# Kernel optimization log

Measured on AMD Instinct MI355X. Metric: run time of the kernel, lower is better.

Reference implementation:

```python
import jax, jax.numpy as jnp
import numpy as np

NUM_HEADS = 12


def _build_mask(N, unseen_size, dtype):
    # Columns for the last `unseen_size` tokens are masked (-inf) for every
    # query row EXCEPT the diagonal entries in that block (each unseen token
    # may attend to itself). Matches the original Python-loop construction.
    idx = jnp.arange(N)
    col_unseen = idx[None, :] >= (N - unseen_size)
    off_diag = idx[:, None] != idx[None, :]
    return jnp.where(col_unseen & off_diag, -jnp.inf, jnp.asarray(0.0, dtype))


def reference(x, w_qkv, w_proj, b_proj, unseen_size):
    B, N, C = x.shape
    H = NUM_HEADS
    d = C // H
    scale = d ** -0.5
    # qkv: (B,N,3C) -> (3,B,H,N,d)
    qkv = (x @ w_qkv.T).reshape(B, N, 3, H, d).transpose(2, 0, 3, 1, 4)
    q, k, v = qkv[0], qkv[1], qkv[2]
    attn = jnp.einsum('bhqd,bhkd->bhqk', q, k) * scale
    attn = attn + _build_mask(N, unseen_size, attn.dtype)  # broadcast (N,N)
    attn = jax.nn.softmax(attn, axis=-1)
    out = jnp.einsum('bhqk,bhkd->bhqd', attn, v)
    out = out.transpose(0, 2, 1, 3).reshape(B, N, C)
    return out @ w_proj.T + b_proj


def setup_inputs() -> dict:
    key = jax.random.key(0)
    k1, k2, k3 = jax.random.split(key, 3)
    B, N, C = 2, 2048, 768
    x = jax.random.normal(k1, (B, N, C), dtype=jnp.float32)
    w_qkv = jax.random.normal(k2, (3 * C, C), dtype=jnp.float32) * (C ** -0.5)
    w_proj = jax.random.normal(k3, (C, C), dtype=jnp.float32) * (C ** -0.5)
    b_proj = jnp.zeros((C,), dtype=jnp.float32)
    return {"x": x, "w_qkv": w_qkv, "w_proj": w_proj, "b_proj": b_proj,
            "unseen_size": 512}
```

## Files before the change

kernel.cpp:

```cpp
#include <hip/hip_runtime.h>
#include <math.h>

#define NH 12
#define DH 64
#define NSEQ 2048
#define NB 2
#define CDIM 768
#define NVIS 1536

typedef _Float16 half8 __attribute__((ext_vector_type(8)));
typedef _Float16 half4 __attribute__((ext_vector_type(4)));
typedef float floatx4 __attribute__((ext_vector_type(4)));

static constexpr size_t SZ_X    = (size_t)NB*NSEQ*CDIM;
static constexpr size_t SZ_WQKV = (size_t)3*CDIM*CDIM;
static constexpr size_t SZ_WP   = (size_t)CDIM*CDIM;
static constexpr size_t SZ_HEAD = (size_t)NB*NH*NSEQ*DH;

#define GLOAD_LDS16(gp, lp) \
  __builtin_amdgcn_global_load_lds((const __attribute__((address_space(1))) void*)(gp), \
                                   (__attribute__((address_space(3))) void*)(lp), 16, 0, 0)

__global__ __launch_bounds__(256) void convert_kernel(
    const float* __restrict__ x, const float* __restrict__ wqkv, const float* __restrict__ wp,
    _Float16* __restrict__ xb, _Float16* __restrict__ wqkvb, _Float16* __restrict__ wpb)
{
  size_t idx = ((size_t)blockIdx.x*256 + threadIdx.x)*4;
  const float* src; _Float16* dst; size_t off;
  if (idx < SZ_X)                        { src = x;    dst = xb;    off = idx; }
  else if (idx < SZ_X+SZ_WQKV)           { src = wqkv; dst = wqkvb; off = idx - SZ_X; }
  else if (idx < SZ_X+SZ_WQKV+SZ_WP)     { src = wp;   dst = wpb;   off = idx - SZ_X - SZ_WQKV; }
  else return;
  float4 v = *reinterpret_cast<const float4*>(src + off);
  _Float16 o[4] = {(_Float16)v.x,(_Float16)v.y,(_Float16)v.z,(_Float16)v.w};
  *reinterpret_cast<uint2*>(dst + off) = *reinterpret_cast<uint2*>(o);
}

template<int MODE, int BN>
__global__ __launch_bounds__(256) void gemm_bt(
    const _Float16* __restrict__ A, const _Float16* __restrict__ Bt,
    const float* __restrict__ bias,
    _Float16* __restrict__ qb, _Float16* __restrict__ kb, _Float16* __restrict__ vb,
    float* __restrict__ outp)
{
  constexpr int K = CDIM;
  constexpr int BM = 128, BK = 32;
  constexpr int MI = (BN == 128) ? 4 : 2;
  constexpr int NI = 4;
  __shared__ _Float16 As[BM*BK];
  __shared__ _Float16 Bs[BN*BK];
  const int tid = threadIdx.x;
  const int lane = tid & 63, wid = tid >> 6;
  const int l15 = lane & 15, quad = lane >> 4;
  const int wm = (BN == 128) ? (wid >> 1)*64 : wid*32;
  const int wn = (BN == 128) ? (wid & 1)*64 : 0;
  const int tileN = blockIdx.x*BN, tileM = blockIdx.y*BM;
  const int lrow = lane >> 2, lchunk = lane & 3;
  const int gcol = ((lchunk ^ (lrow >> 1)) & 3)*8;
  const _Float16* gA0 = A  + (size_t)(tileM + wid*32      + lrow)*K + gcol;
  const _Float16* gA1 = A  + (size_t)(tileM + wid*32 + 16 + lrow)*K + gcol;
  const _Float16* gB0 = Bt + (size_t)(tileN + ((BN==128) ? wid*32 : wid*16) + lrow)*K + gcol;
  const _Float16* gB1 = Bt + (size_t)(tileN + wid*32 + 16 + lrow)*K + gcol;
  _Float16* lA0 = As + (wid*32)*BK;
  _Float16* lA1 = As + (wid*32 + 16)*BK;
  _Float16* lB0 = Bs + ((BN==128) ? wid*32 : wid*16)*BK;
  _Float16* lB1 = Bs + (wid*32 + 16)*BK;
  const int cp = ((quad ^ (l15 >> 1)) & 3)*8;
  floatx4 acc[MI][NI] = {};
  for (int k0 = 0; k0 < K; k0 += BK) {
    __syncthreads();
    GLOAD_LDS16(gA0 + k0, lA0);
    GLOAD_LDS16(gA1 + k0, lA1);
    GLOAD_LDS16(gB0 + k0, lB0);
    if (BN == 128) GLOAD_LDS16(gB1 + k0, lB1);
    __syncthreads();
    half8 af[MI], bfr[NI];
    #pragma unroll
    for (int mi = 0; mi < MI; mi++)
      af[mi] = *reinterpret_cast<const half8*>(&As[(wm + mi*16 + l15)*BK + cp]);
    #pragma unroll
    for (int ni = 0; ni < NI; ni++)
      bfr[ni] = *reinterpret_cast<const half8*>(&Bs[(wn + ni*16 + l15)*BK + cp]);
    #pragma unroll
    for (int mi = 0; mi < MI; mi++)
      #pragma unroll
      for (int ni = 0; ni < NI; ni++)
        acc[mi][ni] = __builtin_amdgcn_mfma_f32_16x16x32_f16(af[mi], bfr[ni], acc[mi][ni], 0,0,0);
  }
  #pragma unroll
  for (int mi = 0; mi < MI; mi++)
    #pragma unroll
    for (int ni = 0; ni < NI; ni++) {
      int n = tileN + wn + ni*16 + l15;
      int m0 = tileM + wm + mi*16 + quad*4;
      if (MODE == 0) {
        int part = n / CDIM, rem = n - part*CDIM;
        int h = rem >> 6, dd = rem & 63;
        int b = m0 >> 11, i0 = m0 & 2047;
        if (part == 2) {
          half4 pk = {(_Float16)acc[mi][ni][0], (_Float16)acc[mi][ni][1],
                      (_Float16)acc[mi][ni][2], (_Float16)acc[mi][ni][3]};
          *reinterpret_cast<half4*>(&vb[(((size_t)b*NH + h)*DH + dd)*NSEQ + i0]) = pk;
        } else {
          _Float16* dst = part ? kb : qb;
          float sc = part ? 1.0f : 0.125f*1.44269504f;
          #pragma unroll
          for (int r = 0; r < 4; r++)
            dst[(((size_t)b*NH + h)*NSEQ + i0 + r)*DH + dd] = (_Float16)(acc[mi][ni][r]*sc);
        }
      } else {
        #pragma unroll
        for (int r = 0; r < 4; r++)
          outp[(size_t)(m0 + r)*CDIM + n] = acc[mi][ni][r] + bias[n];
      }
    }
}

__global__ __launch_bounds__(256, 3) void fa_kernel(
    const _Float16* __restrict__ qg, const _Float16* __restrict__ kg,
    const _Float16* __restrict__ vtg, _Float16* __restrict__ og)
{
  constexpr int LDP = 136;
  __shared__ _Float16 Ps[64*LDP];
  __shared__ float Ls[4*64];
  const int blk = blockIdx.x;
  const int idx = blk >> 3;
  const int bh = (blk & 7)*3 + (idx % 3);
  const int qbase = (idx / 3) * 64;
  const int tid = threadIdx.x;
  const int lane = tid & 63, w = tid >> 6;
  const int l15 = lane & 15, quad = lane >> 4;
  const _Float16* qp  = qg  + (size_t)bh*NSEQ*DH;
  const _Float16* kbp = kg  + (size_t)bh*NSEQ*DH;
  const _Float16* vbp = vtg + (size_t)bh*DH*NSEQ;
  half8 qf[4][2];
  #pragma unroll
  for (int g = 0; g < 4; g++)
    #pragma unroll
    for (int c = 0; c < 2; c++)
      qf[g][c] = *reinterpret_cast<const half8*>(qp + (size_t)(qbase + g*16 + l15)*DH + c*32 + quad*8);
  const _Float16* kRow = kbp + (size_t)(w*16 + l15)*DH + quad*8;
  const _Float16* vRow = vbp + (size_t)(w*16 + l15)*NSEQ + quad*8;
  half8 kc[2][2], vc[2][2];
  #pragma unroll
  for (int s = 0; s < 2; s++)
    #pragma unroll
    for (int c = 0; c < 2; c++) {
      kc[s][c] = *reinterpret_cast<const half8*>(kRow + (size_t)(s*64)*DH + c*32);
      vc[s][c] = *reinterpret_cast<const half8*>(vRow + s*64 + c*32);
    }
  floatx4 o[4] = {};
  float lsum[4] = {0.f, 0.f, 0.f, 0.f};
  for (int t = 0; t < 12; t++) {
    const int tn = (t + 1 < 12) ? t + 1 : 0;
    half8 kn[2][2], vn[2][2];
    #pragma unroll
    for (int s = 0; s < 2; s++)
      #pragma unroll
      for (int c = 0; c < 2; c++) {
        kn[s][c] = *reinterpret_cast<const half8*>(kRow + (size_t)(tn*128 + s*64)*DH + c*32);
        vn[s][c] = *reinterpret_cast<const half8*>(vRow + tn*128 + s*64 + c*32);
      }
    half4 pk[2][4];
    #pragma unroll
    for (int s = 0; s < 2; s++) {
      floatx4 st[4] = {};
      #pragma unroll
      for (int g = 0; g < 4; g++) {
        st[g] = __builtin_amdgcn_mfma_f32_16x16x32_f16(kc[s][0], qf[g][0], st[g], 0,0,0);
        st[g] = __builtin_amdgcn_mfma_f32_16x16x32_f16(kc[s][1], qf[g][1], st[g], 0,0,0);
      }
      #pragma unroll
      for (int g = 0; g < 4; g++) {
        float e0 = __builtin_exp2f(st[g][0]), e1 = __builtin_exp2f(st[g][1]);
        float e2 = __builtin_exp2f(st[g][2]), e3 = __builtin_exp2f(st[g][3]);
        lsum[g] += (e0+e1)+(e2+e3);
        pk[s][g] = half4{(_Float16)e0,(_Float16)e1,(_Float16)e2,(_Float16)e3};
      }
    }
    __syncthreads();
    #pragma unroll
    for (int s = 0; s < 2; s++)
      #pragma unroll
      for (int g = 0; g < 4; g++)
        *reinterpret_cast<half4*>(&Ps[(g*16+l15)*LDP + s*64 + w*16 + quad*4]) = pk[s][g];
    __syncthreads();
    #pragma unroll
    for (int g = 0; g < 4; g++) {
      #pragma unroll
      for (int s = 0; s < 2; s++)
        #pragma unroll
        for (int c = 0; c < 2; c++) {
          half8 pb = *reinterpret_cast<const half8*>(&Ps[(g*16+l15)*LDP + s*64 + c*32 + quad*8]);
          o[g] = __builtin_amdgcn_mfma_f32_16x16x32_f16(vc[s][c], pb, o[g], 0,0,0);
        }
    }
    #pragma unroll
    for (int s = 0; s < 2; s++)
      #pragma unroll
      for (int c = 0; c < 2; c++) { kc[s][c] = kn[s][c]; vc[s][c] = vn[s][c]; }
  }
  #pragma unroll
  for (int g = 0; g < 4; g++) {
    lsum[g] += __shfl_xor(lsum[g], 16);
    lsum[g] += __shfl_xor(lsum[g], 32);
  }
  if (lane < 16) {
    #pragma unroll
    for (int g = 0; g < 4; g++) Ls[w*64 + g*16 + lane] = lsum[g];
  }
  __syncthreads();
  float den[4];
  #pragma unroll
  for (int g = 0; g < 4; g++)
    den[g] = Ls[g*16+l15] + Ls[64+g*16+l15] + Ls[128+g*16+l15] + Ls[192+g*16+l15];
  if (qbase >= NVIS) {
    #pragma unroll
    for (int g = 0; g < 4; g++) {
      half8 kd0 = *reinterpret_cast<const half8*>(kbp + (size_t)(qbase + g*16 + l15)*DH + quad*8);
      half8 kd1 = *reinterpret_cast<const half8*>(kbp + (size_t)(qbase + g*16 + l15)*DH + 32 + quad*8);
      float pd = 0.f;
      #pragma unroll
      for (int j = 0; j < 8; j++)
        pd += (float)qf[g][0][j]*(float)kd0[j] + (float)qf[g][1][j]*(float)kd1[j];
      pd += __shfl_xor(pd, 16);
      pd += __shfl_xor(pd, 32);
      float e = __builtin_exp2f(pd);
      den[g] += e;
      #pragma unroll
      for (int r = 0; r < 4; r++)
        o[g][r] += e * (float)vbp[(size_t)(w*16+quad*4+r)*NSEQ + qbase + g*16 + l15];
    }
  }
  const int b = bh / NH, h = bh - b*NH;
  #pragma unroll
  for (int g = 0; g < 4; g++) {
    float inv = 1.0f / den[g];
    half4 pk = {(_Float16)(o[g][0]*inv), (_Float16)(o[g][1]*inv),
                (_Float16)(o[g][2]*inv), (_Float16)(o[g][3]*inv)};
    size_t oaddr = ((size_t)b*NSEQ + qbase + g*16 + l15)*CDIM + h*DH + w*16 + quad*4;
    *reinterpret_cast<half4*>(&og[oaddr]) = pk;
  }
}

extern "C" void kernel_launch(void* const* d_in, const int* in_sizes, int n_in,
                              void* d_out, int out_size, void* d_ws, size_t ws_size,
                              hipStream_t stream) {
  (void)in_sizes; (void)n_in; (void)out_size; (void)ws_size;
  const float* x     = (const float*)d_in[0];
  const float* wqkv  = (const float*)d_in[1];
  const float* wproj = (const float*)d_in[2];
  const float* bproj = (const float*)d_in[3];

  _Float16* xb    = (_Float16*)d_ws;
  _Float16* wqkvb = xb + SZ_X;
  _Float16* wpb   = wqkvb + SZ_WQKV;
  _Float16* qb    = wpb + SZ_WP;
  _Float16* kb    = qb + SZ_HEAD;
  _Float16* vb    = kb + SZ_HEAD;
  _Float16* ob    = vb + SZ_HEAD;
  float* outp = (float*)d_out;

  size_t total = SZ_X + SZ_WQKV + SZ_WP;
  int cblocks = (int)((total/4 + 255)/256);
  convert_kernel<<<cblocks, 256, 0, stream>>>(x, wqkv, wproj, xb, wqkvb, wpb);
  gemm_bt<0,128><<<dim3(3*CDIM/128, NB*NSEQ/128), 256, 0, stream>>>(xb, wqkvb, nullptr, qb, kb, vb, nullptr);
  fa_kernel<<<NB*NH*(NSEQ/64), 256, 0, stream>>>(qb, kb, vb, ob);
  gemm_bt<1,64><<<dim3(CDIM/64, NB*NSEQ/128), 256, 0, stream>>>(ob, wpb, bproj, nullptr, nullptr, nullptr, outp);
}
```

Baseline: 166.0 us.

## Restructure attention kernel into smaller blocks with double-buffered, software-pipelined P tiles

The flash-attention kernel moves from 256-thread blocks covering 64 queries to 128-thread blocks covering 32 queries, which doubles the grid. P is now double-buffered in shared memory and the loop is skewed, so the QK^T/exp for tile t+1 overlaps the PV product for tile t. This needs only one barrier per iteration instead of two. The aim is to cut barrier stalls and raise occupancy, at the cost of reloading K/V tiles from global memory twice as often across blocks.

```diff
diff --git a/kernel.cpp b/kernel.cpp
--- a/kernel.cpp
+++ b/kernel.cpp
@@ -116,109 +116,147 @@
     }
 }
 
-__global__ __launch_bounds__(256, 3) void fa_kernel(
+__global__ __launch_bounds__(128, 3) void fa_kernel(
     const _Float16* __restrict__ qg, const _Float16* __restrict__ kg,
     const _Float16* __restrict__ vtg, _Float16* __restrict__ og)
 {
-  constexpr int LDP = 136;
-  __shared__ _Float16 Ps[64*LDP];
-  __shared__ float Ls[4*64];
+  constexpr int LDP = 72;
+  __shared__ _Float16 Ps[2][32*LDP];
+  __shared__ float Ls[2*32];
   const int blk = blockIdx.x;
   const int idx = blk >> 3;
   const int bh = (blk & 7)*3 + (idx % 3);
-  const int qbase = (idx / 3) * 64;
+  const int qbase = (idx / 3) * 32;
   const int tid = threadIdx.x;
   const int lane = tid & 63, w = tid >> 6;
   const int l15 = lane & 15, quad = lane >> 4;
   const _Float16* qp  = qg  + (size_t)bh*NSEQ*DH;
   const _Float16* kbp = kg  + (size_t)bh*NSEQ*DH;
   const _Float16* vbp = vtg + (size_t)bh*DH*NSEQ;
-  half8 qf[4][2];
-  #pragma unroll
-  for (int g = 0; g < 4; g++)
+  half8 qf[2][2];
+  #pragma unroll
+  for (int g = 0; g < 2; g++)
     #pragma unroll
     for (int c = 0; c < 2; c++)
       qf[g][c] = *reinterpret_cast<const half8*>(qp + (size_t)(qbase + g*16 + l15)*DH + c*32 + quad*8);
-  const _Float16* kRow = kbp + (size_t)(w*16 + l15)*DH + quad*8;
-  const _Float16* vRow = vbp + (size_t)(w*16 + l15)*NSEQ + quad*8;
-  half8 kc[2][2], vc[2][2];
-  #pragma unroll
-  for (int s = 0; s < 2; s++)
-    #pragma unroll
-    for (int c = 0; c < 2; c++) {
-      kc[s][c] = *reinterpret_cast<const half8*>(kRow + (size_t)(s*64)*DH + c*32);
-      vc[s][c] = *reinterpret_cast<const half8*>(vRow + s*64 + c*32);
+  const _Float16* kRow[2], * vRow[2];
+  #pragma unroll
+  for (int f = 0; f < 2; f++) {
+    kRow[f] = kbp + (size_t)(w*32 + f*16 + l15)*DH + quad*8;
+    vRow[f] = vbp + (size_t)(w*32 + f*16 + l15)*NSEQ + quad*8;
+  }
+  floatx4 o[2][2] = {};
+  float lsum[2] = {0.f, 0.f};
+
+  half8 kc[2][2];
+  #pragma unroll
+  for (int f = 0; f < 2; f++)
+    #pragma unroll
+    for (int c = 0; c < 2; c++)
+      kc[f][c] = *reinterpret_cast<const half8*>(kRow[f] + c*32);
+  #pragma unroll
+  for (int g = 0; g < 2; g++)
+    #pragma unroll
+    for (int f = 0; f < 2; f++) {
+      floatx4 st = {};
+      st = __builtin_amdgcn_mfma_f32_16x16x32_f16(kc[f][0], qf[g][0], st, 0,0,0);
+      st = __builtin_amdgcn_mfma_f32_16x16x32_f16(kc[f][1], qf[g][1], st, 0,0,0);
+      float e0 = __builtin_exp2f(st[0]), e1 = __builtin_exp2f(st[1]);
+      float e2 = __builtin_exp2f(st[2]), e3 = __builtin_exp2f(st[3]);
+      lsum[g] += (e0+e1)+(e2+e3);
+      half4 pk = {(_Float16)e0,(_Float16)e1,(_Float16)e2,(_Float16)e3};
+      *reinterpret_cast<half4*>(&Ps[0][(g*16+l15)*LDP + w*32 + f*16 + quad*4]) = pk;
     }
-  floatx4 o[4] = {};
-  float lsum[4] = {0.f, 0.f, 0.f, 0.f};
-  for (int t = 0; t < 12; t++) {
-    const int tn = (t + 1 < 12) ? t + 1 : 0;
-    half8 kn[2][2], vn[2][2];
-    #pragma unroll
-    for (int s = 0; s < 2; s++)
+  #pragma unroll
+  for (int f = 0; f < 2; f++)
+    #pragma unroll
+    for (int c = 0; c < 2; c++)
+      kc[f][c] = *reinterpret_cast<const half8*>(kRow[f] + (size_t)64*DH + c*32);
+
+  for (int t = 0; t < 23; t++) {
+    half8 vc[2][2];
+    #pragma unroll
+    for (int df = 0; df < 2; df++)
+      #pragma unroll
+      for (int c = 0; c < 2; c++)
+        vc[df][c] = *reinterpret_cast<const half8*>(vRow[df] + t*64 + c*32);
+    const int tk = (t + 2 < 24) ? t + 2 : 0;
+    half8 kn[2][2];
+    #pragma unroll
+    for (int f = 0; f < 2; f++)
+      #pragma unroll
+      for (int c = 0; c < 2; c++)
+        kn[f][c] = *reinterpret_cast<const half8*>(kRow[f] + (size_t)tk*64*DH + c*32);
+    half4 pk[2][2];
+    #pragma unroll
+    for (int g = 0; g < 2; g++)
+      #pragma unroll
+      for (int f = 0; f < 2; f++) {
+        floatx4 st = {};
+        st = __builtin_amdgcn_mfma_f32_16x16x32_f16(kc[f][0], qf[g][0], st, 0,0,0);
+        st = __builtin_amdgcn_mfma_f32_16x16x32_f16(kc[f][1], qf[g][1], st, 0,0,0);
+        float e0 = __builtin_exp2f(st[0]), e1 = __builtin_exp2f(st[1]);
+        float e2 = __builtin_exp2f(st[2]), e3 = __builtin_exp2f(st[3]);
+        lsum[g] += (e0+e1)+(e2+e3);
+        pk[g][f] = half4{(_Float16)e0,(_Float16)e1,(_Float16)e2,(_Float16)e3};
+      }
+    __syncthreads();
+    #pragma unroll
+    for (int g = 0; g < 2; g++)
+      #pragma unroll
+      for (int f = 0; f < 2; f++)
+        *reinterpret_cast<half4*>(&Ps[(t+1)&1][(g*16+l15)*LDP + w*32 + f*16 + quad*4]) = pk[g][f];
+    #pragma unroll
+    for (int g = 0; g < 2; g++)
       #pragma unroll
       for (int c = 0; c < 2; c++) {
-        kn[s][c] = *reinterpret_cast<const half8*>(kRow + (size_t)(tn*128 + s*64)*DH + c*32);
-        vn[s][c] = *reinterpret_cast<const half8*>(vRow + tn*128 + s*64 + c*32);
+        half8 pb = *reinterpret_cast<const half8*>(&Ps[t&1][(g*16+l15)*LDP + c*32 + quad*8]);
+        o[g][0] = __builtin_amdgcn_mfma_f32_16x16x32_f16(vc[0][c], pb, o[g][0], 0,0,0);
+        o[g][1] = __builtin_amdgcn_mfma_f32_16x16x32_f16(vc[1][c], pb, o[g][1], 0,0,0);
       }
-    half4 pk[2][4];
-    #pragma unroll
-    for (int s = 0; s < 2; s++) {
-      floatx4 st[4] = {};
-      #pragma unroll
-      for (int g = 0; g < 4; g++) {
-        st[g] = __builtin_amdgcn_mfma_f32_16x16x32_f16(kc[s][0], qf[g][0], st[g], 0,0,0);
-        st[g] = __builtin_amdgcn_mfma_f32_16x16x32_f16(kc[s][1], qf[g][1], st[g], 0,0,0);
+    #pragma unroll
+    for (int f = 0; f < 2; f++)
+      #pragma unroll
+      for (int c = 0; c < 2; c++)
+        kc[f][c] = kn[f][c];
+  }
+  {
+    half8 vc[2][2];
+    #pragma unroll
+    for (int df = 0; df < 2; df++)
+      #pragma unroll
+      for (int c = 0; c < 2; c++)
+        vc[df][c] = *reinterpret_cast<const half8*>(vRow[df] + 23*64 + c*32);
+    __syncthreads();
+    #pragma unroll
+    for (int g = 0; g < 2; g++)
+      #pragma unroll
+      for (int c = 0; c < 2; c++) {
+        half8 pb = *reinterpret_cast<const half8*>(&Ps[1][(g*16+l15)*LDP + c*32 + quad*8]);
+        o[g][0] = __builtin_amdgcn_mfma_f32_16x16x32_f16(vc[0][c], pb, o[g][0], 0,0,0);
+        o[g][1] = __builtin_amdgcn_mfma_f32_16x16x32_f16(vc[1][c], pb, o[g][1], 0,0,0);
       }
-      #pragma unroll
-      for (int g = 0; g < 4; g++) {
-        float e0 = __builtin_exp2f(st[g][0]), e1 = __builtin_exp2f(st[g][1]);
-        float e2 = __builtin_exp2f(st[g][2]), e3 = __builtin_exp2f(st[g][3]);
-        lsum[g] += (e0+e1)+(e2+e3);
-        pk[s][g] = half4{(_Float16)e0,(_Float16)e1,(_Float16)e2,(_Float16)e3};
-      }
-    }
-    __syncthreads();
-    #pragma unroll
-    for (int s = 0; s < 2; s++)
-      #pragma unroll
-      for (int g = 0; g < 4; g++)
-        *reinterpret_cast<half4*>(&Ps[(g*16+l15)*LDP + s*64 + w*16 + quad*4]) = pk[s][g];
-    __syncthreads();
-    #pragma unroll
-    for (int g = 0; g < 4; g++) {
-      #pragma unroll
-      for (int s = 0; s < 2; s++)
-        #pragma unroll
-        for (int c = 0; c < 2; c++) {
-          half8 pb = *reinterpret_cast<const half8*>(&Ps[(g*16+l15)*LDP + s*64 + c*32 + quad*8]);
-          o[g] = __builtin_amdgcn_mfma_f32_16x16x32_f16(vc[s][c], pb, o[g], 0,0,0);
-        }
-    }
-    #pragma unroll
-    for (int s = 0; s < 2; s++)
-      #pragma unroll
-      for (int c = 0; c < 2; c++) { kc[s][c] = kn[s][c]; vc[s][c] = vn[s][c]; }
-  }
-  #pragma unroll
-  for (int g = 0; g < 4; g++) {
+  }
+  #pragma unroll
+  for (int g = 0; g < 2; g++) {
     lsum[g] += __shfl_xor(lsum[g], 16);
     lsum[g] += __shfl_xor(lsum[g], 32);
   }
   if (lane < 16) {
     #pragma unroll
-    for (int g = 0; g < 4; g++) Ls[w*64 + g*16 + lane] = lsum[g];
+    for (int g = 0; g < 2; g++) Ls[w*32 + g*16 + lane] = lsum[g];
   }
   __syncthreads();
-  float den[4];
-  #pragma unroll
-  for (int g = 0; g < 4; g++)
-    den[g] = Ls[g*16+l15] + Ls[64+g*16+l15] + Ls[128+g*16+l15] + Ls[192+g*16+l15];
+  float den[2];
+  #pragma unroll
+  for (int g = 0; g < 2; g++)
+    den[g] = Ls[g*16+l15] + Ls[32+g*16+l15];
   if (qbase >= NVIS) {
     #pragma unroll
-    for (int g = 0; g < 4; g++) {
-      half8 kd0 = *reinterpret_cast<const half8*>(kbp + (size_t)(qbase + g*16 + l15)*DH + quad*8);
-      half8 kd1 = *reinterpret_cast<const half8*>(kbp + (size_t)(qbase + g*16 + l15)*DH + 32 + quad*8);
+    for (int g = 0; g < 2; g++) {
+      const int q_abs = qbase + g*16 + l15;
+      half8 kd0 = *reinterpret_cast<const half8*>(kbp + (size_t)q_abs*DH + quad*8);
+      half8 kd1 = *reinterpret_cast<const half8*>(kbp + (size_t)q_abs*DH + 32 + quad*8);
       float pd = 0.f;
       #pragma unroll
       for (int j = 0; j < 8; j++)
@@ -228,18 +266,24 @@
       float e = __builtin_exp2f(pd);
       den[g] += e;
       #pragma unroll
-      for (int r = 0; r < 4; r++)
-        o[g][r] += e * (float)vbp[(size_t)(w*16+quad*4+r)*NSEQ + qbase + g*16 + l15];
+      for (int df = 0; df < 2; df++)
+        #pragma unroll
+        for (int r = 0; r < 4; r++)
+          o[g][df][r] += e * (float)vbp[(size_t)(w*32 + df*16 + quad*4 + r)*NSEQ + q_abs];
     }
   }
   const int b = bh / NH, h = bh - b*NH;
   #pragma unroll
-  for (int g = 0; g < 4; g++) {
-    float inv = 1.0f / den[g];
-    half4 pk = {(_Float16)(o[g][0]*inv), (_Float16)(o[g][1]*inv),
-                (_Float16)(o[g][2]*inv), (_Float16)(o[g][3]*inv)};
-    size_t oaddr = ((size_t)b*NSEQ + qbase + g*16 + l15)*CDIM + h*DH + w*16 + quad*4;
-    *reinterpret_cast<half4*>(&og[oaddr]) = pk;
+  for (int g = 0; g < 2; g++) {
+    const float inv = 1.0f / den[g];
+    const int q_abs = qbase + g*16 + l15;
+    #pragma unroll
+    for (int df = 0; df < 2; df++) {
+      half4 pk = {(_Float16)(o[g][df][0]*inv), (_Float16)(o[g][df][1]*inv),
+                  (_Float16)(o[g][df][2]*inv), (_Float16)(o[g][df][3]*inv)};
+      size_t oaddr = ((size_t)b*NSEQ + q_abs)*CDIM + h*DH + w*32 + df*16 + quad*4;
+      *reinterpret_cast<half4*>(&og[oaddr]) = pk;
+    }
   }
 }
 
@@ -265,6 +309,6 @@
   int cblocks = (int)((total/4 + 255)/256);
   convert_kernel<<<cblocks, 256, 0, stream>>>(x, wqkv, wproj, xb, wqkvb, wpb);
   gemm_bt<0,128><<<dim3(3*CDIM/128, NB*NSEQ/128), 256, 0, stream>>>(xb, wqkvb, nullptr, qb, kb, vb, nullptr);
-  fa_kernel<<<NB*NH*(NSEQ/64), 256, 0, stream>>>(qb, kb, vb, ob);
+  fa_kernel<<<NB*NH*(NSEQ/32), 128, 0, stream>>>(qb, kb, vb, ob);
   gemm_bt<1,64><<<dim3(CDIM/64, NB*NSEQ/128), 256, 0, stream>>>(ob, wpb, bproj, nullptr, nullptr, nullptr, outp);
 }
```

New measurement: 188.5 us. 13.5% more time.

## Restructure attention kernel with 32x32 MFMA and register-resident P via lane shuffles

Applied to the files above, without the earlier changes.

The attention kernel moves from 16x16x32 MFMA tiles to 32x32x16 tiles. Each wave now owns a 32-query by 32-key slice, with waves split two ways over queries and two ways over keys. The softmax probabilities are packed with cvt_pkrtz and rearranged across lane halves using shuffles, so the per-iteration LDS round-trip and both __syncthreads in the main loop go away. Partial outputs from the two key-half waves are combined through an LDS buffer at the end, which also transposes the result for coalesced half8 stores. In exchange, the kernel uses more accumulator registers and adds an epilogue reduction, and V fragments are no longer prefetched one iteration ahead.

```diff
diff --git a/kernel.cpp b/kernel.cpp
--- a/kernel.cpp
+++ b/kernel.cpp
@@ -10,7 +10,9 @@
 
 typedef _Float16 half8 __attribute__((ext_vector_type(8)));
 typedef _Float16 half4 __attribute__((ext_vector_type(4)));
+typedef __fp16 fp16x2 __attribute__((ext_vector_type(2)));
 typedef float floatx4 __attribute__((ext_vector_type(4)));
+typedef float floatx16 __attribute__((ext_vector_type(16)));
 
 static constexpr size_t SZ_X    = (size_t)NB*NSEQ*CDIM;
 static constexpr size_t SZ_WQKV = (size_t)3*CDIM*CDIM;
@@ -20,6 +22,12 @@
 #define GLOAD_LDS16(gp, lp) \
   __builtin_amdgcn_global_load_lds((const __attribute__((address_space(1))) void*)(gp), \
                                    (__attribute__((address_space(3))) void*)(lp), 16, 0, 0)
+
+static __device__ __forceinline__ int pack_e2(float a, float b) {
+  union { fp16x2 h; int i; } u;
+  u.h = __builtin_amdgcn_cvt_pkrtz(a, b);
+  return u.i;
+}
 
 __global__ __launch_bounds__(256) void convert_kernel(
     const float* __restrict__ x, const float* __restrict__ wqkv, const float* __restrict__ wp,
@@ -120,126 +128,127 @@
     const _Float16* __restrict__ qg, const _Float16* __restrict__ kg,
     const _Float16* __restrict__ vtg, _Float16* __restrict__ og)
 {
-  constexpr int LDP = 136;
-  __shared__ _Float16 Ps[64*LDP];
-  __shared__ float Ls[4*64];
+  constexpr int LDO = 65;
+  __shared__ float Obuf[64*LDO];
+  __shared__ float Ls[64];
   const int blk = blockIdx.x;
   const int idx = blk >> 3;
   const int bh = (blk & 7)*3 + (idx % 3);
   const int qbase = (idx / 3) * 64;
   const int tid = threadIdx.x;
   const int lane = tid & 63, w = tid >> 6;
-  const int l15 = lane & 15, quad = lane >> 4;
+  const int l31 = lane & 31, hi = lane >> 5;
+  const int qh = w >> 1, kh = w & 1;
   const _Float16* qp  = qg  + (size_t)bh*NSEQ*DH;
   const _Float16* kbp = kg  + (size_t)bh*NSEQ*DH;
   const _Float16* vbp = vtg + (size_t)bh*DH*NSEQ;
-  half8 qf[4][2];
+  const _Float16* qrow = qp + (size_t)(qbase + qh*32 + l31)*DH;
+  half8 qf[4];
   #pragma unroll
-  for (int g = 0; g < 4; g++)
-    #pragma unroll
-    for (int c = 0; c < 2; c++)
-      qf[g][c] = *reinterpret_cast<const half8*>(qp + (size_t)(qbase + g*16 + l15)*DH + c*32 + quad*8);
-  const _Float16* kRow = kbp + (size_t)(w*16 + l15)*DH + quad*8;
-  const _Float16* vRow = vbp + (size_t)(w*16 + l15)*NSEQ + quad*8;
-  half8 kc[2][2], vc[2][2];
+  for (int c = 0; c < 4; c++)
+    qf[c] = *reinterpret_cast<const half8*>(qrow + c*16 + hi*8);
+  const _Float16* kRow  = kbp + (size_t)(kh*32 + l31)*DH;
+  const _Float16* vRow0 = vbp + (size_t)l31*NSEQ + kh*32;
+  const _Float16* vRow1 = vbp + (size_t)(32 + l31)*NSEQ + kh*32;
+  const floatx16 zac = {};
+  floatx16 o0 = {}, o1 = {};
+  float lsum = 0.f;
+  half8 kc[4];
   #pragma unroll
-  for (int s = 0; s < 2; s++)
-    #pragma unroll
-    for (int c = 0; c < 2; c++) {
-      kc[s][c] = *reinterpret_cast<const half8*>(kRow + (size_t)(s*64)*DH + c*32);
-      vc[s][c] = *reinterpret_cast<const half8*>(vRow + s*64 + c*32);
-    }
-  floatx4 o[4] = {};
-  float lsum[4] = {0.f, 0.f, 0.f, 0.f};
-  for (int t = 0; t < 12; t++) {
-    const int tn = (t + 1 < 12) ? t + 1 : 0;
-    half8 kn[2][2], vn[2][2];
-    #pragma unroll
-    for (int s = 0; s < 2; s++)
-      #pragma unroll
-      for (int c = 0; c < 2; c++) {
-        kn[s][c] = *reinterpret_cast<const half8*>(kRow + (size_t)(tn*128 + s*64)*DH + c*32);
-        vn[s][c] = *reinterpret_cast<const half8*>(vRow + tn*128 + s*64 + c*32);
-      }
-    half4 pk[2][4];
-    #pragma unroll
-    for (int s = 0; s < 2; s++) {
-      floatx4 st[4] = {};
-      #pragma unroll
-      for (int g = 0; g < 4; g++) {
-        st[g] = __builtin_amdgcn_mfma_f32_16x16x32_f16(kc[s][0], qf[g][0], st[g], 0,0,0);
-        st[g] = __builtin_amdgcn_mfma_f32_16x16x32_f16(kc[s][1], qf[g][1], st[g], 0,0,0);
-      }
-      #pragma unroll
-      for (int g = 0; g < 4; g++) {
-        float e0 = __builtin_exp2f(st[g][0]), e1 = __builtin_exp2f(st[g][1]);
-        float e2 = __builtin_exp2f(st[g][2]), e3 = __builtin_exp2f(st[g][3]);
-        lsum[g] += (e0+e1)+(e2+e3);
-        pk[s][g] = half4{(_Float16)e0,(_Float16)e1,(_Float16)e2,(_Float16)e3};
-      }
-    }
-    __syncthreads();
-    #pragma unroll
-    for (int s = 0; s < 2; s++)
-      #pragma unroll
-      for (int g = 0; g < 4; g++)
-        *reinterpret_cast<half4*>(&Ps[(g*16+l15)*LDP + s*64 + w*16 + quad*4]) = pk[s][g];
-    __syncthreads();
-    #pragma unroll
-    for (int g = 0; g < 4; g++) {
-      #pragma unroll
-      for (int s = 0; s < 2; s++)
-        #pragma unroll
-        for (int c = 0; c < 2; c++) {
-          half8 pb = *reinterpret_cast<const half8*>(&Ps[(g*16+l15)*LDP + s*64 + c*32 + quad*8]);
-          o[g] = __builtin_amdgcn_mfma_f32_16x16x32_f16(vc[s][c], pb, o[g], 0,0,0);
-        }
-    }
-    #pragma unroll
-    for (int s = 0; s < 2; s++)
-      #pragma unroll
-      for (int c = 0; c < 2; c++) { kc[s][c] = kn[s][c]; vc[s][c] = vn[s][c]; }
-  }
-  #pragma unroll
-  for (int g = 0; g < 4; g++) {
-    lsum[g] += __shfl_xor(lsum[g], 16);
-    lsum[g] += __shfl_xor(lsum[g], 32);
-  }
-  if (lane < 16) {
-    #pragma unroll
-    for (int g = 0; g < 4; g++) Ls[w*64 + g*16 + lane] = lsum[g];
+  for (int c = 0; c < 4; c++)
+    kc[c] = *reinterpret_cast<const half8*>(kRow + c*16 + hi*8);
+  for (int t = 0; t < 24; t++) {
+    const int tk = (t + 1 < 24) ? t + 1 : 0;
+    half8 kn[4];
+    #pragma unroll
+    for (int c = 0; c < 4; c++)
+      kn[c] = *reinterpret_cast<const half8*>(kRow + (size_t)tk*4096 + c*16 + hi*8);
+    half8 vf[2][2];
+    #pragma unroll
+    for (int c2 = 0; c2 < 2; c2++) {
+      vf[0][c2] = *reinterpret_cast<const half8*>(vRow0 + t*64 + c2*16 + hi*8);
+      vf[1][c2] = *reinterpret_cast<const half8*>(vRow1 + t*64 + c2*16 + hi*8);
+    }
+    floatx16 st = __builtin_amdgcn_mfma_f32_32x32x16_f16(kc[0], qf[0], zac, 0,0,0);
+    st = __builtin_amdgcn_mfma_f32_32x32x16_f16(kc[1], qf[1], st, 0,0,0);
+    st = __builtin_amdgcn_mfma_f32_32x32x16_f16(kc[2], qf[2], st, 0,0,0);
+    st = __builtin_amdgcn_mfma_f32_32x32x16_f16(kc[3], qf[3], st, 0,0,0);
+    int dw[8];
+    #pragma unroll
+    for (int i = 0; i < 8; i++) {
+      float e0 = __builtin_exp2f(st[2*i]), e1 = __builtin_exp2f(st[2*i+1]);
+      lsum += e0 + e1;
+      dw[i] = pack_e2(e0, e1);
+    }
+    int pw[8];
+    #pragma unroll
+    for (int i = 0; i < 8; i++) pw[i] = __shfl_xor(dw[i], 32);
+    union { int i[4]; half8 v; } b0u, b1u;
+    b0u.i[0] = hi ? pw[2] : dw[0];  b0u.i[1] = hi ? pw[3] : dw[1];
+    b0u.i[2] = hi ? dw[2] : pw[0];  b0u.i[3] = hi ? dw[3] : pw[1];
+    b1u.i[0] = hi ? pw[6] : dw[4];  b1u.i[1] = hi ? pw[7] : dw[5];
+    b1u.i[2] = hi ? dw[6] : pw[4];  b1u.i[3] = hi ? dw[7] : pw[5];
+    o0 = __builtin_amdgcn_mfma_f32_32x32x16_f16(vf[0][0], b0u.v, o0, 0,0,0);
+    o0 = __builtin_amdgcn_mfma_f32_32x32x16_f16(vf[0][1], b1u.v, o0, 0,0,0);
+    o1 = __builtin_amdgcn_mfma_f32_32x32x16_f16(vf[1][0], b0u.v, o1, 0,0,0);
+    o1 = __builtin_amdgcn_mfma_f32_32x32x16_f16(vf[1][1], b1u.v, o1, 0,0,0);
+    #pragma unroll
+    for (int c = 0; c < 4; c++) kc[c] = kn[c];
+  }
+  lsum += __shfl_xor(lsum, 32);
+  if (kh == 1) {
+    #pragma unroll
+    for (int r = 0; r < 16; r++) {
+      const int d = (r & 3) + 8*(r >> 2) + 4*hi;
+      Obuf[d*LDO + qh*32 + l31]        = o0[r];
+      Obuf[(32 + d)*LDO + qh*32 + l31] = o1[r];
+    }
+    if (lane < 32) Ls[qh*32 + l31] = lsum;
   }
   __syncthreads();
-  float den[4];
-  #pragma unroll
-  for (int g = 0; g < 4; g++)
-    den[g] = Ls[g*16+l15] + Ls[64+g*16+l15] + Ls[128+g*16+l15] + Ls[192+g*16+l15];
-  if (qbase >= NVIS) {
-    #pragma unroll
-    for (int g = 0; g < 4; g++) {
-      half8 kd0 = *reinterpret_cast<const half8*>(kbp + (size_t)(qbase + g*16 + l15)*DH + quad*8);
-      half8 kd1 = *reinterpret_cast<const half8*>(kbp + (size_t)(qbase + g*16 + l15)*DH + 32 + quad*8);
+  if (kh == 0) {
+    float den = lsum + Ls[qh*32 + l31];
+    if (qbase >= NVIS) {
+      const int q_abs = qbase + qh*32 + l31;
+      const _Float16* krow = kbp + (size_t)q_abs*DH;
       float pd = 0.f;
       #pragma unroll
-      for (int j = 0; j < 8; j++)
-        pd += (float)qf[g][0][j]*(float)kd0[j] + (float)qf[g][1][j]*(float)kd1[j];
-      pd += __shfl_xor(pd, 16);
+      for (int c = 0; c < 4; c++) {
+        half8 kd = *reinterpret_cast<const half8*>(krow + c*16 + hi*8);
+        #pragma unroll
+        for (int j = 0; j < 8; j++) pd += (float)qf[c][j]*(float)kd[j];
+      }
       pd += __shfl_xor(pd, 32);
       float e = __builtin_exp2f(pd);
-      den[g] += e;
+      den += e;
       #pragma unroll
-      for (int r = 0; r < 4; r++)
-        o[g][r] += e * (float)vbp[(size_t)(w*16+quad*4+r)*NSEQ + qbase + g*16 + l15];
-    }
-  }
-  const int b = bh / NH, h = bh - b*NH;
-  #pragma unroll
-  for (int g = 0; g < 4; g++) {
-    float inv = 1.0f / den[g];
-    half4 pk = {(_Float16)(o[g][0]*inv), (_Float16)(o[g][1]*inv),
-                (_Float16)(o[g][2]*inv), (_Float16)(o[g][3]*inv)};
-    size_t oaddr = ((size_t)b*NSEQ + qbase + g*16 + l15)*CDIM + h*DH + w*16 + quad*4;
-    *reinterpret_cast<half4*>(&og[oaddr]) = pk;
+      for (int r = 0; r < 16; r++) {
+        const int d = (r & 3) + 8*(r >> 2) + 4*hi;
+        o0[r] += e * (float)vbp[(size_t)d*NSEQ + q_abs];
+        o1[r] += e * (float)vbp[(size_t)(32 + d)*NSEQ + q_abs];
+      }
+    }
+    const float inv = 1.0f / den;
+    #pragma unroll
+    for (int r = 0; r < 16; r++) {
+      const int d = (r & 3) + 8*(r >> 2) + 4*hi;
+      Obuf[d*LDO + qh*32 + l31]        = (o0[r] + Obuf[d*LDO + qh*32 + l31]) * inv;
+      Obuf[(32 + d)*LDO + qh*32 + l31] = (o1[r] + Obuf[(32 + d)*LDO + qh*32 + l31]) * inv;
+    }
+  }
+  __syncthreads();
+  {
+    const int q64 = tid >> 2, dseg = (tid & 3)*16;
+    const int b = bh / NH, h = bh - b*NH;
+    half8 h0, h1;
+    #pragma unroll
+    for (int j = 0; j < 8; j++) {
+      h0[j] = (_Float16)Obuf[(dseg + j)*LDO + q64];
+      h1[j] = (_Float16)Obuf[(dseg + 8 + j)*LDO + q64];
+    }
+    size_t base = ((size_t)b*NSEQ + qbase + q64)*CDIM + h*DH + dseg;
+    *reinterpret_cast<half8*>(&og[base])     = h0;
+    *reinterpret_cast<half8*>(&og[base + 8]) = h1;
   }
 }
 
```

Measured after the change: 186.8 us. 12.5% more time.
